# Kernel optimization log

Hardware: AMD Instinct MI355X
Metric: run time of the kernel (lower is better)

## Reference

```python
import jax, jax.numpy as jnp
import numpy as np

# Per-channel class frequencies from the original module (23 AU channels)
_W = np.array([0.0012597430655963838, 0.0004919313290455535, 0.0021106513104319356,
               0.0007678117365508301, 0.004719881670572202, 0.000372272357115554,
               0.029090425620315438, 0.010056339432617042, 0.0034817436971298467,
               0.0003057951504877765, 0.003995280118329428, 8.808229878180519e-05,
               0.012070598793438699, 0.016788818533845208, 0.0017832510677901316,
               0.0008758371973209686, 0.0005933090691529143, 0.0031992155689617922,
               0.003212511010287348, 0.0016685778863572154, 0.0009356666832859684,
               0.0010985358395240233, 0.00103372056306194], dtype=np.float32)
_WEIGHT_0 = 1.0 / (_W + 1.0)        # used when target == 0
_WEIGHT_1 = 1.0 - _WEIGHT_0          # used when target == 1

B, C = 1000000, 23

def setup_inputs() -> dict:
    key = jax.random.key(0)
    k1, k2 = jax.random.split(key)
    # probabilities strictly inside (0,1) so log terms stay finite
    x = jax.random.uniform(k1, (B, C), dtype=jnp.float32) * 0.98 + 0.01
    labels = jax.random.randint(k2, (B, C), 0, 2, dtype=jnp.int32)
    return {"x": x, "labels": labels}

def reference(x, labels):
    # target = (labels > 0).float(); the eq(999) mask in the original is computed but unused
    target = (labels > 0).astype(x.dtype)
    w0 = jnp.asarray(_WEIGHT_0, dtype=x.dtype)  # [C]
    w1 = jnp.asarray(_WEIGHT_1, dtype=x.dtype)  # [C]
    # per-element weight: 1/weight_0[ch] if target==0 else 1/weight_1[ch]
    w = jnp.where(target == 0, 1.0 / w0, 1.0 / w1)  # [B, C] via broadcast
    bce = -(target * jnp.log(x) + (1.0 - target) * jnp.log(1.0 - x))
    loss = jnp.sum(w * bce)
    n, c = x.shape
    return loss / (n * c)
```

## Files before the change

### kernel.cpp

```cpp
#include <hip/hip_runtime.h>

#define NCH 23
#define U 8
#define TILE_V4 (64 * U)

typedef float fvec4 __attribute__((ext_vector_type(4)));
typedef int   ivec4 __attribute__((ext_vector_type(4)));

constexpr float c_W[NCH] = {
    0.0012597430655963838f, 0.0004919313290455535f, 0.0021106513104319356f,
    0.0007678117365508301f, 0.004719881670572202f,  0.000372272357115554f,
    0.029090425620315438f,  0.010056339432617042f,  0.0034817436971298467f,
    0.0003057951504877765f, 0.003995280118329428f,  8.808229878180519e-05f,
    0.012070598793438699f,  0.016788818533845208f,  0.0017832510677901316f,
    0.0008758371973209686f, 0.0005933090691529143f, 0.0031992155689617922f,
    0.003212511010287348f,  0.0016685778863572154f, 0.0009356666832859684f,
    0.0010985358395240233f, 0.00103372056306194f
};
constexpr float NEG_LN2 = -0.69314718055994530942f;

struct Tabs { float w[2 * NCH]; };
constexpr Tabs make_tabs() {
    Tabs t{};
    for (int c = 0; c < NCH; ++c) {
        float w0 = 1.0f / (c_W[c] + 1.0f);
        float w1 = 1.0f - w0;
        t.w[c]       = (1.0f / w0) * NEG_LN2;
        t.w[NCH + c] = (1.0f / w1) * NEG_LN2;
    }
    return t;
}
__constant__ Tabs d_tabs = make_tabs();

__device__ __forceinline__ unsigned wrap23(unsigned c) {
    return c >= NCH ? c - NCH : c;
}

__device__ __forceinline__ void elem(float xx, int lab, unsigned c,
                                     const float* s_wt, float& acc) {
    bool t  = lab > 0;
    float v = t ? xx : 1.0f - xx;
    float w = s_wt[c + (t ? NCH : 0u)];
    acc = __builtin_fmaf(w, __log2f(v), acc);
}

__global__ __launch_bounds__(256) void bce_reduce_kernel(
        const fvec4* __restrict__ x4, const ivec4* __restrict__ l4,
        double* __restrict__ partial, unsigned n4 ) {
    __shared__ float s_wt[2 * NCH];
    if (threadIdx.x < 2 * NCH) s_wt[threadIdx.x] = d_tabs.w[threadIdx.x];
    __syncthreads();

    const unsigned gtid     = blockIdx.x * blockDim.x + threadIdx.x;
    const unsigned nthreads = gridDim.x * blockDim.x;
    const unsigned lane     = threadIdx.x & 63u;
    const unsigned wid      = gtid >> 6;
    const unsigned nwaves   = nthreads >> 6;
    const unsigned ntiles   = n4 / TILE_V4;

    float acc0 = 0.0f, acc1 = 0.0f;

    for (unsigned T = wid; T < ntiles; T += nwaves) {
        const fvec4* px = x4 + (size_t)T * TILE_V4 + lane;
        const ivec4* pl = l4 + (size_t)T * TILE_V4 + lane;
        fvec4 xv[U];
        ivec4 lv[U];
        #pragma unroll
        for (int j = 0; j < U; ++j)
            xv[j] = __builtin_nontemporal_load(px + 64u * j);
        #pragma unroll
        for (int j = 0; j < U; ++j)
            lv[j] = __builtin_nontemporal_load(pl + 64u * j);
        __builtin_amdgcn_sched_barrier(0);

        const unsigned cb = (T + 4u * lane) % NCH;
        #pragma unroll
        for (int j = 0; j < U; ++j) {
            unsigned c = wrap23(cb + (3u * j) % NCH);
            float& a = (j & 1) ? acc1 : acc0;
            elem(xv[j].x, lv[j].x, c, s_wt, a); c = wrap23(c + 1);
            elem(xv[j].y, lv[j].y, c, s_wt, a); c = wrap23(c + 1);
            elem(xv[j].z, lv[j].z, c, s_wt, a); c = wrap23(c + 1);
            elem(xv[j].w, lv[j].w, c, s_wt, a);
        }
    }

    for (unsigned v = ntiles * TILE_V4 + gtid; v < n4; v += nthreads) {
        fvec4 xv = __builtin_nontemporal_load(x4 + v);
        ivec4 lv = __builtin_nontemporal_load(l4 + v);
        unsigned c = (4u * v) % NCH;
        elem(xv.x, lv.x, c, s_wt, acc0); c = wrap23(c + 1);
        elem(xv.y, lv.y, c, s_wt, acc0); c = wrap23(c + 1);
        elem(xv.z, lv.z, c, s_wt, acc0); c = wrap23(c + 1);
        elem(xv.w, lv.w, c, s_wt, acc0);
    }

    float acc = acc0 + acc1;

    #pragma unroll
    for (int off = 32; off > 0; off >>= 1) acc += __shfl_down(acc, off, 64);
    __shared__ float s_part[4];
    const int wave = threadIdx.x >> 6;
    if ((threadIdx.x & 63) == 0) s_part[wave] = acc;
    __syncthreads();
    if (threadIdx.x == 0) {
        float s = s_part[0] + s_part[1] + s_part[2] + s_part[3];
        atomicAdd(partial, (double)s);
    }
}

__global__ void bce_finalize_kernel(const double* __restrict__ partial,
                                    float* __restrict__ out, unsigned n) {
    out[0] = (float)(partial[0] / (double)n);
}

extern "C" void kernel_launch(void* const* d_in, const int* in_sizes, int n_in,
                              void* d_out, int out_size, void* d_ws, size_t ws_size,
                              hipStream_t stream) {
    const float* x      = (const float*)d_in[0];
    const int*   labels = (const int*)d_in[1];
    float*       out    = (float*)d_out;
    double*      acc    = (double*)d_ws;
    unsigned n  = (unsigned)in_sizes[0];
    unsigned n4 = n >> 2;

    (void)hipMemsetAsync(acc, 0, sizeof(double), stream);

    const int block = 256;
    const int grid  = 2048;
    bce_reduce_kernel<<<grid, block, 0, stream>>>(
        (const fvec4*)x, (const ivec4*)labels, acc, n4);
    bce_finalize_kernel<<<1, 1, 0, stream>>>(acc, out, n);
}
```

Measured before the change: 192.6 us.

## Stage inputs through LDS with direct global-to-LDS loads per block step

Replaces per-wave unrolled nontemporal vector loads with block-wide global_load_lds transfers of 2048 elements of x and labels into shared memory, followed by barrier-separated compute. The intent is to use the direct-to-LDS path to cut register pressure and VMEM-to-VGPR traffic. It adds two block barriers per step and has no double buffering, which reduces the loads in flight per wave and may expose memory latency.

```diff
diff --git a/kernel.cpp b/kernel.cpp
--- a/kernel.cpp
+++ b/kernel.cpp
@@ -1,8 +1,8 @@
 #include <hip/hip_runtime.h>
 
 #define NCH 23
-#define U 8
-#define TILE_V4 (64 * U)
+#define STEP_ELEMS 2048
+#define XCHUNK 1024
 
 typedef float fvec4 __attribute__((ext_vector_type(4)));
 typedef int   ivec4 __attribute__((ext_vector_type(4)));
@@ -44,55 +44,57 @@
     acc = __builtin_fmaf(w, __log2f(v), acc);
 }
 
+__device__ __forceinline__ void gld_lds16(const void* g, void* l) {
+    __builtin_amdgcn_global_load_lds(
+        (const __attribute__((address_space(1))) void*)g,
+        (__attribute__((address_space(3))) void*)l, 16, 0, 0);
+}
+
 __global__ __launch_bounds__(256) void bce_reduce_kernel(
-        const fvec4* __restrict__ x4, const ivec4* __restrict__ l4,
-        double* __restrict__ partial, unsigned n4 ) {
+        const float* __restrict__ x, const int* __restrict__ labels,
+        double* __restrict__ partial, unsigned n) {
     __shared__ float s_wt[2 * NCH];
-    if (threadIdx.x < 2 * NCH) s_wt[threadIdx.x] = d_tabs.w[threadIdx.x];
-    __syncthreads();
+    __shared__ float sx[STEP_ELEMS];
+    __shared__ int   sl[STEP_ELEMS];
 
-    const unsigned gtid     = blockIdx.x * blockDim.x + threadIdx.x;
-    const unsigned nthreads = gridDim.x * blockDim.x;
-    const unsigned lane     = threadIdx.x & 63u;
-    const unsigned wid      = gtid >> 6;
-    const unsigned nwaves   = nthreads >> 6;
-    const unsigned ntiles   = n4 / TILE_V4;
+    const unsigned tid = threadIdx.x;
+    if (tid < 2 * NCH) s_wt[tid] = d_tabs.w[tid];
 
+    const unsigned nsteps = n / STEP_ELEMS;
     float acc0 = 0.0f, acc1 = 0.0f;
 
-    for (unsigned T = wid; T < ntiles; T += nwaves) {
-        const fvec4* px = x4 + (size_t)T * TILE_V4 + lane;
-        const ivec4* pl = l4 + (size_t)T * TILE_V4 + lane;
-        fvec4 xv[U];
-        ivec4 lv[U];
-        #pragma unroll
-        for (int j = 0; j < U; ++j)
-            xv[j] = __builtin_nontemporal_load(px + 64u * j);
-        #pragma unroll
-        for (int j = 0; j < U; ++j)
-            lv[j] = __builtin_nontemporal_load(pl + 64u * j);
-        __builtin_amdgcn_sched_barrier(0);
+    for (unsigned g = blockIdx.x; g < nsteps; g += gridDim.x) {
+        const unsigned ebase = g * STEP_ELEMS;
+        gld_lds16(x + ebase + tid * 4u,               sx + tid * 4u);
+        gld_lds16(x + ebase + XCHUNK + tid * 4u,      sx + XCHUNK + tid * 4u);
+        gld_lds16(labels + ebase + tid * 4u,          sl + tid * 4u);
+        gld_lds16(labels + ebase + XCHUNK + tid * 4u, sl + XCHUNK + tid * 4u);
+        __syncthreads();
 
-        const unsigned cb = (T + 4u * lane) % NCH;
-        #pragma unroll
-        for (int j = 0; j < U; ++j) {
-            unsigned c = wrap23(cb + (3u * j) % NCH);
-            float& a = (j & 1) ? acc1 : acc0;
-            elem(xv[j].x, lv[j].x, c, s_wt, a); c = wrap23(c + 1);
-            elem(xv[j].y, lv[j].y, c, s_wt, a); c = wrap23(c + 1);
-            elem(xv[j].z, lv[j].z, c, s_wt, a); c = wrap23(c + 1);
-            elem(xv[j].w, lv[j].w, c, s_wt, a);
-        }
+        fvec4 xv0 = *(const fvec4*)(sx + tid * 4u);
+        ivec4 lv0 = *(const ivec4*)(sl + tid * 4u);
+        fvec4 xv1 = *(const fvec4*)(sx + XCHUNK + tid * 4u);
+        ivec4 lv1 = *(const ivec4*)(sl + XCHUNK + tid * 4u);
+
+        unsigned c0 = (ebase + tid * 4u) % NCH;
+        unsigned c  = c0;
+        elem(xv0.x, lv0.x, c, s_wt, acc0); c = wrap23(c + 1);
+        elem(xv0.y, lv0.y, c, s_wt, acc0); c = wrap23(c + 1);
+        elem(xv0.z, lv0.z, c, s_wt, acc0); c = wrap23(c + 1);
+        elem(xv0.w, lv0.w, c, s_wt, acc0);
+        c = wrap23(c0 + 12u);
+        elem(xv1.x, lv1.x, c, s_wt, acc1); c = wrap23(c + 1);
+        elem(xv1.y, lv1.y, c, s_wt, acc1); c = wrap23(c + 1);
+        elem(xv1.z, lv1.z, c, s_wt, acc1); c = wrap23(c + 1);
+        elem(xv1.w, lv1.w, c, s_wt, acc1);
+
+        __syncthreads();
     }
 
-    for (unsigned v = ntiles * TILE_V4 + gtid; v < n4; v += nthreads) {
-        fvec4 xv = __builtin_nontemporal_load(x4 + v);
-        ivec4 lv = __builtin_nontemporal_load(l4 + v);
-        unsigned c = (4u * v) % NCH;
-        elem(xv.x, lv.x, c, s_wt, acc0); c = wrap23(c + 1);
-        elem(xv.y, lv.y, c, s_wt, acc0); c = wrap23(c + 1);
-        elem(xv.z, lv.z, c, s_wt, acc0); c = wrap23(c + 1);
-        elem(xv.w, lv.w, c, s_wt, acc0);
+    const unsigned gtid     = blockIdx.x * blockDim.x + tid;
+    const unsigned nthreads = gridDim.x * blockDim.x;
+    for (unsigned i = nsteps * STEP_ELEMS + gtid; i < n; i += nthreads) {
+        elem(x[i], labels[i], i % NCH, s_wt, acc0);
     }
 
     float acc = acc0 + acc1;
@@ -121,14 +123,12 @@
     const int*   labels = (const int*)d_in[1];
     float*       out    = (float*)d_out;
     double*      acc    = (double*)d_ws;
-    unsigned n  = (unsigned)in_sizes[0];
-    unsigned n4 = n >> 2;
+    unsigned n = (unsigned)in_sizes[0];
 
     (void)hipMemsetAsync(acc, 0, sizeof(double), stream);
 
     const int block = 256;
     const int grid  = 2048;
-    bce_reduce_kernel<<<grid, block, 0, stream>>>(
-        (const fvec4*)x, (const ivec4*)labels, acc, n4);
+    bce_reduce_kernel<<<grid, block, 0, stream>>>(x, labels, acc, n);
     bce_finalize_kernel<<<1, 1, 0, stream>>>(acc, out, n);
 }
```

Result: slower. 198.7 us (+3.2%).
